# Kernel tuning notes

Measured on AMD Instinct MI355X. Metric: run time of the kernel, lower is better.

## Reference

```python
import jax, jax.numpy as jnp
import numpy as np

N = 2
GRIDS = [(512, 512), (256, 256), (128, 128), (64, 64), (32, 32)]
STRIDES = [4, 8, 16, 32, 64]
SIZES = [32, 64, 128, 256, 512]
ASPECTS = (0.5, 1.0, 2.0)
A = len(ASPECTS)
IMG_H = IMG_W = 2048
PRE_NMS = 1000      # pre_nms_top_n['testing']
POST_NMS = 1000     # post_nms_top_n['testing']
NMS_THRESH = 0.7
SCORE_THRESH = 0.0
MIN_SIZE = 1e-3
BBOX_XFORM_CLIP = float(np.log(1000.0 / 16.0))  # torchvision BoxCoder clamp


def _make_anchors():
    """AnchorGenerator.grid_anchors for each level; returns list of [H*W*A, 4]."""
    ar = jnp.asarray(ASPECTS, jnp.float32)
    hr = jnp.sqrt(ar)
    wr = 1.0 / hr
    levels = []
    for (gh, gw), s, size in zip(GRIDS, STRIDES, SIZES):
        ws = wr * size
        hs = hr * size
        base = jnp.round(jnp.stack([-ws, -hs, ws, hs], 1) / 2.0)  # [A,4]
        sx = (jnp.arange(gw) * s).astype(jnp.float32)
        sy = (jnp.arange(gh) * s).astype(jnp.float32)
        yy, xx = jnp.meshgrid(sy, sx, indexing='ij')
        shifts = jnp.stack([xx.ravel(), yy.ravel(), xx.ravel(), yy.ravel()], 1)
        levels.append((shifts[:, None, :] + base[None, :, :]).reshape(-1, 4))
    return levels


def _flatten_obj(o):
    # permute_and_flatten with C=1: [N,A,H,W] -> [N, H*W*A]
    n, ac, h, w = o.shape
    return o.reshape(n, ac, 1, h, w).transpose(0, 3, 4, 1, 2).reshape(n, -1)


def _flatten_box(b):
    # permute_and_flatten with C=4: [N,A*4,H,W] -> [N, H*W*A, 4]
    n, a4, h, w = b.shape
    return b.reshape(n, a4 // 4, 4, h, w).transpose(0, 3, 4, 1, 2).reshape(n, -1, 4)


def _decode(deltas, anchors):
    # BoxCoder.decode with weights (1,1,1,1); deltas [N,M,4], anchors [M,4]
    wa = anchors[:, 2] - anchors[:, 0]
    ha = anchors[:, 3] - anchors[:, 1]
    cxa = anchors[:, 0] + 0.5 * wa
    cya = anchors[:, 1] + 0.5 * ha
    dx, dy = deltas[..., 0], deltas[..., 1]
    dw = jnp.minimum(deltas[..., 2], BBOX_XFORM_CLIP)
    dh = jnp.minimum(deltas[..., 3], BBOX_XFORM_CLIP)
    cx = dx * wa + cxa
    cy = dy * ha + cya
    w = jnp.exp(dw) * wa
    h = jnp.exp(dh) * ha
    return jnp.stack([cx - 0.5 * w, cy - 0.5 * h, cx + 0.5 * w, cy + 0.5 * h], -1)


def _nms_select(boxes, scores, n_out, thresh):
    """Greedy NMS returning fixed n_out (index, valid) pairs. boxes [K,4]."""
    area = jnp.maximum(boxes[:, 2] - boxes[:, 0], 0.0) * jnp.maximum(boxes[:, 3] - boxes[:, 1], 0.0)

    def step(s, _):
        i = jnp.argmax(s)
        valid = s[i] > -jnp.inf
        b = boxes[i]
        lt = jnp.maximum(boxes[:, :2], b[:2])
        rb = jnp.minimum(boxes[:, 2:], b[2:])
        wh = jnp.maximum(rb - lt, 0.0)
        inter = wh[:, 0] * wh[:, 1]
        iou = inter / (area + area[i] - inter + 1e-9)
        s = jnp.where(iou > thresh, -jnp.inf, s).at[i].set(-jnp.inf)
        return s, (i, valid)

    _, (idx, valid) = jax.lax.scan(step, scores, None, length=n_out)
    return idx, valid


def _rpn_forward(objs, dts):
    anchors = _make_anchors()
    b_all, s_all, l_all = [], [], []
    for li, (o, d, a) in enumerate(zip(objs, dts, anchors)):
        of = _flatten_obj(o)            # [N, HWA]
        df = _flatten_box(d)            # [N, HWA, 4]
        props = _decode(df, a)          # [N, HWA, 4]
        k = min(PRE_NMS, of.shape[1])
        ts, ti = jax.lax.top_k(of, k)   # top-k on raw objectness (per level)
        b_all.append(jnp.take_along_axis(props, ti[..., None], 1))
        s_all.append(ts)
        l_all.append(jnp.full((of.shape[0], k), float(li), jnp.float32))
    boxes = jnp.concatenate(b_all, 1)   # [N, K, 4]
    raw = jnp.concatenate(s_all, 1)     # [N, K]
    lvl = jnp.concatenate(l_all, 1)     # [N, K]

    def per_image(bx, rs, lv):
        sc = jax.nn.sigmoid(rs)
        x1 = jnp.clip(bx[:, 0], 0.0, IMG_W)
        y1 = jnp.clip(bx[:, 1], 0.0, IMG_H)
        x2 = jnp.clip(bx[:, 2], 0.0, IMG_W)
        y2 = jnp.clip(bx[:, 3], 0.0, IMG_H)
        bx = jnp.stack([x1, y1, x2, y2], 1)
        keep = ((x2 - x1) >= MIN_SIZE) & ((y2 - y1) >= MIN_SIZE) & (sc > SCORE_THRESH)
        ms = jnp.where(keep, sc, -jnp.inf)
        off = lv * (IMG_W + IMG_H + 1.0)  # batched_nms level offset
        idx, valid = _nms_select(jax.lax.stop_gradient(bx + off[:, None]),
                                 jax.lax.stop_gradient(ms), POST_NMS, NMS_THRESH)
        v = valid.astype(bx.dtype)
        ob = bx[idx] * v[:, None]
        os = sc[idx] * v
        return jnp.concatenate([ob, os[:, None]], 1)  # [POST_NMS, 5]

    return jax.vmap(per_image)(boxes, raw, lvl)       # [N, POST_NMS, 5]


def setup_inputs() -> dict:
    key = jax.random.key(0)
    ks = jax.random.split(key, 10)
    inp = {}
    for i, (gh, gw) in enumerate(GRIDS):
        inp[f"obj{i}"] = jax.random.normal(ks[i], (N, A, gh, gw), jnp.float32)
        inp[f"box{i}"] = jax.random.normal(ks[5 + i], (N, A * 4, gh, gw), jnp.float32) * 0.5
    return inp


def reference(obj0, obj1, obj2, obj3, obj4, box0, box1, box2, box3, box4):
    return _rpn_forward([obj0, obj1, obj2, obj3, obj4],
                        [box0, box1, box2, box3, box4])
```

## Files before the change

kernel.cpp:

```cpp
#include <hip/hip_runtime.h>
#include <cmath>

#pragma clang fp contract(off)

typedef unsigned int u32;
typedef unsigned short u16;
typedef unsigned long long u64;

#define K_PER_LVL 1000
#define KTOT 5000
#define NIMG 2
#define BINS 16384
#define BIN_SHIFT 18
#define SEGW (BINS / 256)
#define EQ_CAP 2048
#define ECAP 32768
#define LECAP 24576
#define CBUF 1024
#define RNK_IB 512
#define RNK_JB 250
#define RNK_NJ (KTOT / RNK_JB)
#define RNK_TILES 200
#define EDGE_TILES 820

__constant__ int c_LG[5] = {512, 256, 128, 64, 32};
__constant__ int c_LS[5] = {4, 8, 16, 32, 64};
__constant__ int c_LZ[5] = {32, 64, 128, 256, 512};
__constant__ int c_LM[5] = {786432, 196608, 49152, 12288, 3072};

struct Ptrs { const float* o[5]; const float* b[5]; };

__device__ inline u32 fkey(float f) {
    u32 u = __float_as_uint(f);
    return (u & 0x80000000u) ? ~u : (u | 0x80000000u);
}

__device__ inline void featOne(const Ptrs& P, int p, int s, int m,
                               u64* __restrict__ key64, float* __restrict__ csc,
                               float* __restrict__ cbox, float* __restrict__ cobox) {
    int n = p / 5, l = p % 5;
    int G = c_LG[l], S = c_LS[l], Z = c_LZ[l];
    int gg = G * G;
    int a = m % 3; int pix = m / 3; int h = pix / G; int w = pix - h * G;

    const float ars[3] = {0.5f, 1.0f, 2.0f};
    float ar = ars[a];
    float hr = sqrtf(ar), wr = 1.0f / hr;
    float wsz = wr * (float)Z, hsz = hr * (float)Z;
    float bx1 = rintf(-0.5f * wsz), by1 = rintf(-0.5f * hsz);
    float bx2 = rintf(0.5f * wsz),  by2 = rintf(0.5f * hsz);
    float sx = (float)(w * S), sy = (float)(h * S);
    float ax1 = sx + bx1, ay1 = sy + by1, ax2 = sx + bx2, ay2 = sy + by2;
    float wa = ax2 - ax1, ha = ay2 - ay1;
    float cxa = ax1 + 0.5f * wa, cya = ay1 + 0.5f * ha;

    const float* bb = P.b[l] + (size_t)n * 12 * gg;
    float dx = bb[(a * 4 + 0) * gg + pix];
    float dy = bb[(a * 4 + 1) * gg + pix];
    const float CLIPV = 4.135166556742356f;
    float dw = fminf(bb[(a * 4 + 2) * gg + pix], CLIPV);
    float dh = fminf(bb[(a * 4 + 3) * gg + pix], CLIPV);
    float cx = dx * wa + cxa, cy = dy * ha + cya;
    float ww = expf(dw) * wa, hh = expf(dh) * ha;
    float x1 = cx - 0.5f * ww, y1 = cy - 0.5f * hh;
    float x2 = cx + 0.5f * ww, y2 = cy + 0.5f * hh;
    x1 = fminf(fmaxf(x1, 0.f), 2048.f);
    y1 = fminf(fmaxf(y1, 0.f), 2048.f);
    x2 = fminf(fmaxf(x2, 0.f), 2048.f);
    y2 = fminf(fmaxf(y2, 0.f), 2048.f);

    float raw = P.o[l][(size_t)n * 3 * gg + a * gg + pix];
    float sc = 1.0f / (1.0f + expf(-raw));
    bool keep = (x2 - x1 >= 1e-3f) && (y2 - y1 >= 1e-3f) && (sc > 0.0f);

    int slot = n * KTOT + l * K_PER_LVL + s;
    u32 tb = ((u32)l << 20) | (u32)m;
    u32 kk = keep ? fkey(raw) : 0u;
    key64[slot] = ((u64)kk << 23) | (u64)(tb ^ 0x7FFFFFu);

    csc[slot] = keep ? sc : -INFINITY;
    cbox[slot * 4 + 0] = x1; cbox[slot * 4 + 1] = y1;
    cbox[slot * 4 + 2] = x2; cbox[slot * 4 + 3] = y2;
    float off = 4097.0f * (float)l;
    cobox[slot * 4 + 0] = x1 + off; cobox[slot * 4 + 1] = y1 + off;
    cobox[slot * 4 + 2] = x2 + off; cobox[slot * 4 + 3] = y2 + off;
}

__global__ __launch_bounds__(256) void k_zero(u32* __restrict__ z, int nwords) {
    int i = blockIdx.x * 256 + threadIdx.x;
    int stride = gridDim.x * 256;
    for (; i < nwords; i += stride) z[i] = 0;
}

__global__ __launch_bounds__(256) void k_hist(Ptrs P, u32* __restrict__ hist) {
    int p = blockIdx.y; int l = p % 5; int n = p / 5;
    int M4 = c_LM[l] >> 2;
    const float4* base = (const float4*)(P.o[l] + (size_t)n * c_LM[l]);
    __shared__ u32 lh[BINS];
    for (int i = threadIdx.x; i < BINS; i += 256) lh[i] = 0;
    __syncthreads();
    int stride = gridDim.x * 256;
    for (int i = blockIdx.x * 256 + threadIdx.x; i < M4; i += stride) {
        float4 v = base[i];
        atomicAdd(&lh[fkey(v.x) >> BIN_SHIFT], 1u);
        atomicAdd(&lh[fkey(v.y) >> BIN_SHIFT], 1u);
        atomicAdd(&lh[fkey(v.z) >> BIN_SHIFT], 1u);
        atomicAdd(&lh[fkey(v.w) >> BIN_SHIFT], 1u);
    }
    __syncthreads();
    for (int i = threadIdx.x; i < BINS; i += 256) {
        u32 c = lh[i];
        if (c) atomicAdd(&hist[p * BINS + i], c);
    }
}

__global__ __launch_bounds__(256) void k_resolve(const u32* __restrict__ hist,
                                                 int* __restrict__ binB, int* __restrict__ kneed,
                                                 int* __restrict__ g0) {
    int p = blockIdx.x, t = threadIdx.x;
    __shared__ u32 seg[256];
    __shared__ u32 tail[SEGW];
    __shared__ int sgS; __shared__ u32 GS;
    u32 s = 0;
    const u32* hb = hist + p * BINS;
    int base = t * SEGW;
    for (int q = 0; q < SEGW; ++q) s += hb[base + q];
    seg[t] = s;
    __syncthreads();
    if (t == 0) {
        u32 G = 0; int sg = 255;
        for (; sg > 0; --sg) {
            if (G + seg[sg] >= (u32)K_PER_LVL) break;
            G += seg[sg];
        }
        sgS = sg; GS = G;
    }
    __syncthreads();
    int sg = sgS;
    if (t < SEGW) tail[t] = hb[sg * SEGW + t];
    __syncthreads();
    if (t == 0) {
        u32 G = GS; int B = sg * SEGW;
        for (int b = SEGW - 1; b >= 0; --b) {
            u32 c = tail[b];
            if (G + c >= (u32)K_PER_LVL) { B = sg * SEGW + b; break; }
            G += c;
        }
        binB[p] = B;
        kneed[p] = K_PER_LVL - (int)G;
        g0[p] = (int)G;
    }
}

__global__ __launch_bounds__(256) void k_compact(Ptrs P, const int* __restrict__ binB,
                                                 u32* gcnt, u32* ecnt,
                                                 int* __restrict__ sel, u64* __restrict__ eq) {
    int p = blockIdx.y; int l = p % 5; int n = p / 5;
    int M4 = c_LM[l] >> 2; int gg = c_LM[l] / 3;
    const float4* base = (const float4*)(P.o[l] + (size_t)n * c_LM[l]);
    int B = binB[p];
    __shared__ u32 lsel[CBUF];
    __shared__ u64 leq[CBUF];
    __shared__ u32 cSel, cEq, baseSel, baseEq;
    if (threadIdx.x == 0) { cSel = 0; cEq = 0; }
    __syncthreads();
    int stride = gridDim.x * 256;
    for (int i4 = blockIdx.x * 256 + threadIdx.x; i4 < M4; i4 += stride) {
        float4 v = base[i4];
        float vv[4] = {v.x, v.y, v.z, v.w};
        #pragma unroll
        for (int q = 0; q < 4; ++q) {
            u32 k = fkey(vv[q]);
            int bin = (int)(k >> BIN_SHIFT);
            if (bin < B) continue;
            int i = i4 * 4 + q;
            int a = i / gg; int pix = i - a * gg; int m = pix * 3 + a;
            if (bin > B) {
                u32 t = atomicAdd(&cSel, 1u);
                if (t < CBUF) lsel[t] = (u32)m;
                else { u32 pos = atomicAdd(&gcnt[p], 1u); sel[p * K_PER_LVL + pos] = m; }
            } else {
                u64 pk = ((u64)k << 20) | (u64)(0xFFFFFu ^ (u32)m);
                u32 t = atomicAdd(&cEq, 1u);
                if (t < CBUF) leq[t] = pk;
                else { u32 e = atomicAdd(&ecnt[p], 1u); if (e < EQ_CAP) eq[(size_t)p * EQ_CAP + e] = pk; }
            }
        }
    }
    __syncthreads();
    if (threadIdx.x == 0) {
        u32 ns = cSel < CBUF ? cSel : CBUF;
        u32 ne = cEq < CBUF ? cEq : CBUF;
        baseSel = ns ? atomicAdd(&gcnt[p], ns) : 0u;
        baseEq  = ne ? atomicAdd(&ecnt[p], ne) : 0u;
    }
    __syncthreads();
    u32 ns = cSel < CBUF ? cSel : CBUF;
    u32 ne = cEq < CBUF ? cEq : CBUF;
    for (u32 i = threadIdx.x; i < ns; i += 256) sel[p * K_PER_LVL + baseSel + i] = (int)lsel[i];
    for (u32 i = threadIdx.x; i < ne; i += 256) {
        u32 slot = baseEq + i;
        if (slot < EQ_CAP) eq[(size_t)p * EQ_CAP + slot] = leq[i];
    }
}

__global__ __launch_bounds__(256) void k_eqfeat(Ptrs P, const u32* __restrict__ ecnt,
                       const int* __restrict__ kneed, const int* __restrict__ g0,
                       const u64* __restrict__ eq, const int* __restrict__ sel,
                       u64* __restrict__ key64, float* __restrict__ csc,
                       float* __restrict__ cbox, float* __restrict__ cobox) {
    int b = blockIdx.x, t = threadIdx.x;
    if (b < 10) {
        int p = b;
        int E = (int)ecnt[p]; if (E > EQ_CAP) E = EQ_CAP;
        int KF = kneed[p]; int G0 = g0[p];
        __shared__ u64 a[EQ_CAP];
        for (int i = t; i < E; i += 256) a[i] = eq[(size_t)p * EQ_CAP + i];
        __syncthreads();
        u64 mine[8]; int rk[8];
        #pragma unroll
        for (int q = 0; q < 8; ++q) {
            int i = t + q * 256;
            mine[q] = (i < E) ? a[i] : 0ULL;
            rk[q] = 0;
        }
        for (int j = 0; j < E; ++j) {
            u64 v = a[j];
            #pragma unroll
            for (int q = 0; q < 8; ++q) rk[q] += (v > mine[q]) ? 1 : 0;
        }
        #pragma unroll
        for (int q = 0; q < 8; ++q) {
            int i = t + q * 256;
            if (i < E && rk[q] < KF) {
                int m = (int)(0xFFFFFu ^ (u32)(mine[q] & 0xFFFFFu));
                featOne(P, p, G0 + rk[q], m, key64, csc, cbox, cobox);
            }
        }
    } else {
        for (int idx = (b - 10) * 256 + t; idx < 10 * K_PER_LVL; idx += 40 * 256) {
            int p = idx / K_PER_LVL, s = idx - p * K_PER_LVL;
            if (s < g0[p]) featOne(P, p, s, sel[p * K_PER_LVL + s], key64, csc, cbox, cobox);
        }
    }
}

__global__ __launch_bounds__(256) void k_redge(const u64* __restrict__ key64, u32* __restrict__ rpart,
                                               const float* __restrict__ cobox,
                                               u32* __restrict__ gE, u32* __restrict__ gPairs) {
    int n = blockIdx.y;
    int x = blockIdx.x;
    __shared__ u64 kj[RNK_JB];
    __shared__ float cb[64][4];
    if (x < RNK_TILES) {
        int i0 = (x / 20) * RNK_IB;
        int j0 = (x % 20) * RNK_JB;
        const u64* kb = key64 + (size_t)n * KTOT;
        for (int t = threadIdx.x; t < RNK_JB; t += 256) kj[t] = kb[j0 + t];
        __syncthreads();
        int i1 = i0 + threadIdx.x, i2 = i1 + 256;
        u64 k1 = (i1 < KTOT) ? kb[i1] : ~0ULL;
        u64 k2 = (i2 < KTOT) ? kb[i2] : ~0ULL;
        u32 r1 = 0, r2 = 0;
        #pragma unroll 10
        for (int j = 0; j < RNK_JB; ++j) {
            u64 v = kj[j];
            r1 += (v > k1) ? 1u : 0u;
            r2 += (v > k2) ? 1u : 0u;
        }
        u32* rp = rpart + (size_t)(x % 20) * (NIMG * KTOT) + n * KTOT;
        if (i1 < KTOT) rp[i1] = r1;
        if (i2 < KTOT) rp[i2] = r2;
        return;
    }
    int e = x - RNK_TILES, bi = 0;
    while (true) { int c = 79 - 4 * bi; if (e < c) break; e -= c; ++bi; }
    int bj = 4 * bi + e;
    int i = bi * 256 + threadIdx.x;
    int j0 = bj * 64;
    if (threadIdx.x < 64) {
        int jl = j0 + threadIdx.x;
        if (jl < KTOT) {
            cb[threadIdx.x][0] = cobox[(size_t)(n * KTOT + jl) * 4 + 0];
            cb[threadIdx.x][1] = cobox[(size_t)(n * KTOT + jl) * 4 + 1];
            cb[threadIdx.x][2] = cobox[(size_t)(n * KTOT + jl) * 4 + 2];
            cb[threadIdx.x][3] = cobox[(size_t)(n * KTOT + jl) * 4 + 3];
        } else {
            cb[threadIdx.x][0] = 0.f; cb[threadIdx.x][1] = 0.f;
            cb[threadIdx.x][2] = 0.f; cb[threadIdx.x][3] = 0.f;
        }
    }
    __syncthreads();
    if (i >= KTOT) return;
    float x1 = cobox[(size_t)(n * KTOT + i) * 4 + 0];
    float y1 = cobox[(size_t)(n * KTOT + i) * 4 + 1];
    float x2 = cobox[(size_t)(n * KTOT + i) * 4 + 2];
    float y2 = cobox[(size_t)(n * KTOT + i) * 4 + 3];
    float areai = fmaxf(x2 - x1, 0.f) * fmaxf(y2 - y1, 0.f);
    int lim = KTOT - j0; if (lim > 64) lim = 64;
    for (int jj = 0; jj < lim; ++jj) {
        int j = j0 + jj;
        if (j <= i) continue;
        float bx1 = cb[jj][0], by1 = cb[jj][1], bx2 = cb[jj][2], by2 = cb[jj][3];
        float areaj = fmaxf(bx2 - bx1, 0.f) * fmaxf(by2 - by1, 0.f);
        float ltx = fmaxf(x1, bx1), lty = fmaxf(y1, by1);
        float rbx = fminf(x2, bx2), rby = fminf(y2, by2);
        float iw = fmaxf(rbx - ltx, 0.f), ih = fmaxf(rby - lty, 0.f);
        float inter = iw * ih;
        float iou = inter / (areai + areaj - inter + 1e-9f);
        if (iou > 0.7f) {
            u32 pos = atomicAdd(&gE[n], 1u);
            if (pos < ECAP) gPairs[(size_t)n * ECAP + pos] = ((u32)i << 13) | (u32)j;
        }
    }
}

__global__ __launch_bounds__(256) void k_scat(const u32* __restrict__ rpart, const float* __restrict__ csc,
                       const float* __restrict__ cbox,
                       float* __restrict__ ssc, float* __restrict__ sbox, u32* __restrict__ rankArr) {
    int n = blockIdx.y;
    int i = blockIdx.x * 256 + threadIdx.x;
    if (i >= KTOT) return;
    int idx = n * KTOT + i;
    u32 rank = 0;
    #pragma unroll
    for (int jb = 0; jb < RNK_NJ; ++jb) rank += rpart[(size_t)jb * (NIMG * KTOT) + idx];
    rankArr[idx] = rank;
    int src = idx, dst = n * KTOT + (int)rank;
    ssc[dst] = csc[src];
    sbox[dst * 4 + 0] = cbox[src * 4 + 0]; sbox[dst * 4 + 1] = cbox[src * 4 + 1];
    sbox[dst * 4 + 2] = cbox[src * 4 + 2]; sbox[dst * 4 + 3] = cbox[src * 4 + 3];
}

__global__ __launch_bounds__(256, 1) void k_nms(const float* __restrict__ ssc,
                      const float* __restrict__ sbox, const u32* __restrict__ rankArr,
                      const u32* __restrict__ gE, u32* __restrict__ gPairs,
                      u16* __restrict__ gEdges, float* __restrict__ out) {
    int n = blockIdx.x, tid = threadIdx.x;
    int lane = tid & 63, wv = tid >> 6;
    __shared__ u32 cnt[KTOT];
    __shared__ u32 offs[KTOT + 1];
    __shared__ u16 edges[LECAP];
    __shared__ u32 rem32[160];
    __shared__ u32 colLo[64], colHi[64];
    __shared__ u32 scanb[256];
    __shared__ int picksS;

    for (int i = tid; i < KTOT; i += 256) cnt[i] = 0;
    if (tid < 160) rem32[tid] = 0xFFFFFFFFu;
    __syncthreads();
    for (int w = wv; w < 79; w += 4) {
        int i = w * 64 + lane;
        bool dead = (i >= KTOT) || !(ssc[n * KTOT + i] > -INFINITY);
        u64 db = __ballot(dead);
        if (lane == 0) { rem32[2 * w] = (u32)db; rem32[2 * w + 1] = (u32)(db >> 32); }
    }
    __syncthreads();

    int E = (int)gE[n]; if (E > ECAP) E = ECAP;
    for (int k = tid; k < E; k += 256) {
        u32 p = gPairs[(size_t)n * ECAP + k];
        u32 ra = rankArr[n * KTOT + (p >> 13)], rb = rankArr[n * KTOT + (p & 0x1FFFu)];
        u32 src = ra < rb ? ra : rb, dst = ra < rb ? rb : ra;
        gPairs[(size_t)n * ECAP + k] = (src << 13) | dst;
        atomicAdd(&cnt[src], 1u);
    }
    __syncthreads();
    u32 s = 0; int base = tid * 20;
    if (tid < 250) for (int q = 0; q < 20; ++q) s += cnt[base + q];
    scanb[tid] = s;
    __syncthreads();
    for (int off = 1; off < 256; off <<= 1) {
        u32 v = (tid >= off) ? scanb[tid - off] : 0;
        __syncthreads();
        scanb[tid] += v;
        __syncthreads();
    }
    u32 tbase = (tid == 0) ? 0u : scanb[tid - 1];
    if (tid < 250) {
        u32 run = tbase;
        for (int q = 0; q < 20; ++q) { offs[base + q] = run; run += cnt[base + q]; }
    }
    if (tid == 0) offs[KTOT] = scanb[255];
    __syncthreads();
    for (int i = tid; i < KTOT; i += 256) cnt[i] = 0;
    __syncthreads();
    for (int k = tid; k < E; k += 256) {
        u32 p = gPairs[(size_t)n * ECAP + k];
        u32 src = p >> 13, dst = p & 0x1FFFu;
        u32 slot = offs[src] + atomicAdd(&cnt[src], 1u);
        if (slot < LECAP) edges[slot] = (u16)dst;
        else gEdges[(size_t)n * ECAP + slot] = (u16)dst;
    }
    __syncthreads();

    if (wv == 0) {
        int picks = 0;
        for (int w = 0; w < 79 && picks < 1000; ++w) {
            u64 rw = ((u64)rem32[2 * w + 1] << 32) | rem32[2 * w];
            u64 alive = ~rw;
            if (alive == 0ULL) continue;
            int c = w * 64 + lane;
            bool amAlive = ((alive >> lane) & 1ULL) != 0ULL;
            int e0 = 0, e1 = 0;
            if (amAlive) { e0 = (int)offs[c]; e1 = (int)offs[c + 1]; }
            colLo[lane] = 0; colHi[lane] = 0;
            bool anyIntra = false;
            for (int k = e0; k < e1; ++k) {
                int dst = (k < LECAP) ? (int)edges[k] : (int)gEdges[(size_t)n * ECAP + k];
                if ((dst >> 6) == w) {
                    if (lane < 32) atomicOr(&colLo[dst & 63], 1u << lane);
                    else           atomicOr(&colHi[dst & 63], 1u << (lane - 32));
                    anyIntra = true;
                }
            }
            u64 cm;
            if (__ballot(anyIntra) == 0ULL) {
                cm = alive;
            } else {
                u64 col = ((u64)colHi[lane] << 32) | colLo[lane];
                cm = 0ULL;
                u64 remb = alive;
                while (remb) {
                    int e = __builtin_ctzll(remb);
                    remb &= remb - 1ULL;
                    u64 ce = __shfl(col, e);
                    if ((cm & ce) == 0ULL) cm |= (1ULL << e);
                }
            }
            int allowed = 1000 - picks;
            int ncom = __popcll(cm);
            while (ncom > allowed) { cm &= ~(1ULL << (63 - __clzll(cm))); --ncom; }
            if ((cm >> lane) & 1ULL) {
                int pos = picks + (int)__popcll(cm & ((1ULL << lane) - 1ULL));
                const float* bp = &sbox[(size_t)(n * KTOT + c) * 4];
                float* op = &out[(n * 1000 + pos) * 5];
                op[0] = bp[0]; op[1] = bp[1]; op[2] = bp[2]; op[3] = bp[3];
                op[4] = ssc[n * KTOT + c];
                for (int k = e0; k < e1; ++k) {
                    int dst = (k < LECAP) ? (int)edges[k] : (int)gEdges[(size_t)n * ECAP + k];
                    atomicOr(&rem32[dst >> 5], 1u << (dst & 31));
                }
            }
            picks += ncom;
        }
        if (lane == 0) picksS = picks;
    }
    __syncthreads();
    int picksF = picksS;
    int basec = (n * 1000 + picksF) * 5, cntz = (1000 - picksF) * 5;
    for (int t = tid; t < cntz; t += 256) out[basec + t] = 0.f;
}

constexpr size_t OFF_HIST   = 0;
constexpr size_t OFF_GCNT   = OFF_HIST + 10 * BINS * 4;
constexpr size_t OFF_ECNT   = OFF_GCNT + 64;
constexpr size_t OFF_GEC    = OFF_ECNT + 64;
constexpr size_t ZERO_WORDS = (10 * BINS * 4 + 192) / 4;
constexpr size_t OFF_BINB   = OFF_GEC + 64;
constexpr size_t OFF_KNEED  = OFF_BINB + 64;
constexpr size_t OFF_G0     = OFF_KNEED + 64;
constexpr size_t OFF_SEL    = OFF_G0 + 64;
constexpr size_t OFF_EQ     = OFF_SEL + 10 * K_PER_LVL * 4;
constexpr size_t OFF_KEY64  = OFF_EQ + (size_t)10 * EQ_CAP * 8;
constexpr size_t OFF_CSC    = OFF_KEY64 + (size_t)NIMG * KTOT * 8;
constexpr size_t OFF_CBOX   = OFF_CSC + (size_t)NIMG * KTOT * 4;
constexpr size_t OFF_COBOX  = OFF_CBOX + (size_t)NIMG * KTOT * 16;
constexpr size_t OFF_SSC    = OFF_COBOX + (size_t)NIMG * KTOT * 16;
constexpr size_t OFF_SBOX   = OFF_SSC + (size_t)NIMG * KTOT * 4;
constexpr size_t OFF_RANK   = OFF_SBOX + (size_t)NIMG * KTOT * 16;
constexpr size_t OFF_PAIRS  = OFF_RANK + (size_t)NIMG * KTOT * 4;
constexpr size_t OFF_ESPILL = OFF_PAIRS + (size_t)NIMG * ECAP * 4;
constexpr size_t OFF_RPART  = OFF_ESPILL + (size_t)NIMG * ECAP * 2;
constexpr size_t WS_NEEDED  = OFF_RPART + (size_t)RNK_NJ * NIMG * KTOT * 4;

extern "C" void kernel_launch(void* const* d_in, const int* in_sizes, int n_in,
                              void* d_out, int out_size, void* d_ws, size_t ws_size,
                              hipStream_t stream) {
    if (ws_size < WS_NEEDED) return;

    bool dictOrder = (in_sizes[1] > in_sizes[0]);
    Ptrs P;
    for (int l = 0; l < 5; ++l) {
        P.o[l] = (const float*)d_in[dictOrder ? (2 * l)     : l];
        P.b[l] = (const float*)d_in[dictOrder ? (2 * l + 1) : (5 + l)];
    }
    char* ws = (char*)d_ws;
    u32*   hist   = (u32*)(ws + OFF_HIST);
    u32*   gcnt   = (u32*)(ws + OFF_GCNT);
    u32*   ecnt   = (u32*)(ws + OFF_ECNT);
    u32*   gec    = (u32*)(ws + OFF_GEC);
    int*   binB   = (int*)(ws + OFF_BINB);
    int*   kneed  = (int*)(ws + OFF_KNEED);
    int*   g0     = (int*)(ws + OFF_G0);
    int*   sel    = (int*)(ws + OFF_SEL);
    u64*   eq     = (u64*)(ws + OFF_EQ);
    u64*   key64  = (u64*)(ws + OFF_KEY64);
    float* csc    = (float*)(ws + OFF_CSC);
    float* cbox   = (float*)(ws + OFF_CBOX);
    float* cobox  = (float*)(ws + OFF_COBOX);
    float* ssc    = (float*)(ws + OFF_SSC);
    float* sbox   = (float*)(ws + OFF_SBOX);
    u32*   rankA  = (u32*)(ws + OFF_RANK);
    u32*   pairs  = (u32*)(ws + OFF_PAIRS);
    u16*   espill = (u16*)(ws + OFF_ESPILL);
    u32*   rpart  = (u32*)(ws + OFF_RPART);
    float* out    = (float*)d_out;

    k_zero<<<dim3(64), 256, 0, stream>>>(hist, (int)ZERO_WORDS);
    k_hist<<<dim3(32, 10), 256, 0, stream>>>(P, hist);
    k_resolve<<<10, 256, 0, stream>>>(hist, binB, kneed, g0);
    k_compact<<<dim3(64, 10), 256, 0, stream>>>(P, binB, gcnt, ecnt, sel, eq);
    k_eqfeat<<<50, 256, 0, stream>>>(P, ecnt, kneed, g0, eq, sel, key64, csc, cbox, cobox);
    k_redge<<<dim3(RNK_TILES + EDGE_TILES, NIMG), 256, 0, stream>>>(key64, rpart, cobox, gec, pairs);
    k_scat<<<dim3((KTOT + 255) / 256, NIMG), 256, 0, stream>>>(rpart, csc, cbox, ssc, sbox, rankA);
    k_nms<<<NIMG, 256, 0, stream>>>(ssc, sbox, rankA, gec, pairs, espill, out);
}
```

Baseline: 195.9 us.

## Accumulate ranks atomically and drop scatter kernel via inverse permutation in NMS

Rank tiles now atomically add their partial counts into a zeroed rank array instead of writing per-tile partials. This removes the separate k_scat kernel and its partial-rank buffer. k_nms builds an inverse permutation in shared memory and gathers scores and boxes from the unsorted compacted arrays. The change saves one kernel launch and a pass over memory, at the cost of global atomics and indirect gathers inside the single-block-per-image NMS kernel.

```diff
diff --git a/kernel.cpp b/kernel.cpp
--- a/kernel.cpp
+++ b/kernel.cpp
@@ -245,7 +245,7 @@
     }
 }
 
-__global__ __launch_bounds__(256) void k_redge(const u64* __restrict__ key64, u32* __restrict__ rpart,
+__global__ __launch_bounds__(256) void k_redge(const u64* __restrict__ key64, u32* __restrict__ rankArr,
                                                const float* __restrict__ cobox,
                                                u32* __restrict__ gE, u32* __restrict__ gPairs) {
     int n = blockIdx.y;
@@ -268,9 +268,8 @@
             r1 += (v > k1) ? 1u : 0u;
             r2 += (v > k2) ? 1u : 0u;
         }
-        u32* rp = rpart + (size_t)(x % 20) * (NIMG * KTOT) + n * KTOT;
-        if (i1 < KTOT) rp[i1] = r1;
-        if (i2 < KTOT) rp[i2] = r2;
+        if (i1 < KTOT && r1) atomicAdd(&rankArr[n * KTOT + i1], r1);
+        if (i2 < KTOT && r2) atomicAdd(&rankArr[n * KTOT + i2], r2);
         return;
     }
     int e = x - RNK_TILES, bi = 0;
@@ -315,25 +314,8 @@
     }
 }
 
-__global__ __launch_bounds__(256) void k_scat(const u32* __restrict__ rpart, const float* __restrict__ csc,
-                       const float* __restrict__ cbox,
-                       float* __restrict__ ssc, float* __restrict__ sbox, u32* __restrict__ rankArr) {
-    int n = blockIdx.y;
-    int i = blockIdx.x * 256 + threadIdx.x;
-    if (i >= KTOT) return;
-    int idx = n * KTOT + i;
-    u32 rank = 0;
-    #pragma unroll
-    for (int jb = 0; jb < RNK_NJ; ++jb) rank += rpart[(size_t)jb * (NIMG * KTOT) + idx];
-    rankArr[idx] = rank;
-    int src = idx, dst = n * KTOT + (int)rank;
-    ssc[dst] = csc[src];
-    sbox[dst * 4 + 0] = cbox[src * 4 + 0]; sbox[dst * 4 + 1] = cbox[src * 4 + 1];
-    sbox[dst * 4 + 2] = cbox[src * 4 + 2]; sbox[dst * 4 + 3] = cbox[src * 4 + 3];
-}
-
-__global__ __launch_bounds__(256, 1) void k_nms(const float* __restrict__ ssc,
-                      const float* __restrict__ sbox, const u32* __restrict__ rankArr,
+__global__ __launch_bounds__(256, 1) void k_nms(const float* __restrict__ csc,
+                      const float* __restrict__ cbox, const u32* __restrict__ rankArr,
                       const u32* __restrict__ gE, u32* __restrict__ gPairs,
                       u16* __restrict__ gEdges, float* __restrict__ out) {
     int n = blockIdx.x, tid = threadIdx.x;
@@ -341,6 +323,7 @@
     __shared__ u32 cnt[KTOT];
     __shared__ u32 offs[KTOT + 1];
     __shared__ u16 edges[LECAP];
+    __shared__ u16 invL[KTOT];
     __shared__ u32 rem32[160];
     __shared__ u32 colLo[64], colHi[64];
     __shared__ u32 scanb[256];
@@ -348,10 +331,11 @@
 
     for (int i = tid; i < KTOT; i += 256) cnt[i] = 0;
     if (tid < 160) rem32[tid] = 0xFFFFFFFFu;
+    for (int i = tid; i < KTOT; i += 256) invL[rankArr[n * KTOT + i]] = (u16)i;
     __syncthreads();
     for (int w = wv; w < 79; w += 4) {
         int i = w * 64 + lane;
-        bool dead = (i >= KTOT) || !(ssc[n * KTOT + i] > -INFINITY);
+        bool dead = (i >= KTOT) || !(csc[n * KTOT + (int)invL[i]] > -INFINITY);
         u64 db = __ballot(dead);
         if (lane == 0) { rem32[2 * w] = (u32)db; rem32[2 * w + 1] = (u32)(db >> 32); }
     }
@@ -433,10 +417,11 @@
             while (ncom > allowed) { cm &= ~(1ULL << (63 - __clzll(cm))); --ncom; }
             if ((cm >> lane) & 1ULL) {
                 int pos = picks + (int)__popcll(cm & ((1ULL << lane) - 1ULL));
-                const float* bp = &sbox[(size_t)(n * KTOT + c) * 4];
+                int orig = (int)invL[c];
+                const float* bp = &cbox[(size_t)(n * KTOT + orig) * 4];
                 float* op = &out[(n * 1000 + pos) * 5];
                 op[0] = bp[0]; op[1] = bp[1]; op[2] = bp[2]; op[3] = bp[3];
-                op[4] = ssc[n * KTOT + c];
+                op[4] = csc[n * KTOT + orig];
                 for (int k = e0; k < e1; ++k) {
                     int dst = (k < LECAP) ? (int)edges[k] : (int)gEdges[(size_t)n * ECAP + k];
                     atomicOr(&rem32[dst >> 5], 1u << (dst & 31));
@@ -456,8 +441,9 @@
 constexpr size_t OFF_GCNT   = OFF_HIST + 10 * BINS * 4;
 constexpr size_t OFF_ECNT   = OFF_GCNT + 64;
 constexpr size_t OFF_GEC    = OFF_ECNT + 64;
-constexpr size_t ZERO_WORDS = (10 * BINS * 4 + 192) / 4;
-constexpr size_t OFF_BINB   = OFF_GEC + 64;
+constexpr size_t OFF_RANK   = OFF_GEC + 64;
+constexpr size_t ZERO_WORDS = (10 * BINS * 4 + 192 + (size_t)NIMG * KTOT * 4) / 4;
+constexpr size_t OFF_BINB   = OFF_RANK + (size_t)NIMG * KTOT * 4;
 constexpr size_t OFF_KNEED  = OFF_BINB + 64;
 constexpr size_t OFF_G0     = OFF_KNEED + 64;
 constexpr size_t OFF_SEL    = OFF_G0 + 64;
@@ -466,13 +452,9 @@
 constexpr size_t OFF_CSC    = OFF_KEY64 + (size_t)NIMG * KTOT * 8;
 constexpr size_t OFF_CBOX   = OFF_CSC + (size_t)NIMG * KTOT * 4;
 constexpr size_t OFF_COBOX  = OFF_CBOX + (size_t)NIMG * KTOT * 16;
-constexpr size_t OFF_SSC    = OFF_COBOX + (size_t)NIMG * KTOT * 16;
-constexpr size_t OFF_SBOX   = OFF_SSC + (size_t)NIMG * KTOT * 4;
-constexpr size_t OFF_RANK   = OFF_SBOX + (size_t)NIMG * KTOT * 16;
-constexpr size_t OFF_PAIRS  = OFF_RANK + (size_t)NIMG * KTOT * 4;
+constexpr size_t OFF_PAIRS  = OFF_COBOX + (size_t)NIMG * KTOT * 16;
 constexpr size_t OFF_ESPILL = OFF_PAIRS + (size_t)NIMG * ECAP * 4;
-constexpr size_t OFF_RPART  = OFF_ESPILL + (size_t)NIMG * ECAP * 2;
-constexpr size_t WS_NEEDED  = OFF_RPART + (size_t)RNK_NJ * NIMG * KTOT * 4;
+constexpr size_t WS_NEEDED  = OFF_ESPILL + (size_t)NIMG * ECAP * 2;
 
 extern "C" void kernel_launch(void* const* d_in, const int* in_sizes, int n_in,
                               void* d_out, int out_size, void* d_ws, size_t ws_size,
@@ -490,6 +472,7 @@
     u32*   gcnt   = (u32*)(ws + OFF_GCNT);
     u32*   ecnt   = (u32*)(ws + OFF_ECNT);
     u32*   gec    = (u32*)(ws + OFF_GEC);
+    u32*   rankA  = (u32*)(ws + OFF_RANK);
     int*   binB   = (int*)(ws + OFF_BINB);
     int*   kneed  = (int*)(ws + OFF_KNEED);
     int*   g0     = (int*)(ws + OFF_G0);
@@ -499,12 +482,8 @@
     float* csc    = (float*)(ws + OFF_CSC);
     float* cbox   = (float*)(ws + OFF_CBOX);
     float* cobox  = (float*)(ws + OFF_COBOX);
-    float* ssc    = (float*)(ws + OFF_SSC);
-    float* sbox   = (float*)(ws + OFF_SBOX);
-    u32*   rankA  = (u32*)(ws + OFF_RANK);
     u32*   pairs  = (u32*)(ws + OFF_PAIRS);
     u16*   espill = (u16*)(ws + OFF_ESPILL);
-    u32*   rpart  = (u32*)(ws + OFF_RPART);
     float* out    = (float*)d_out;
 
     k_zero<<<dim3(64), 256, 0, stream>>>(hist, (int)ZERO_WORDS);
@@ -512,7 +491,6 @@
     k_resolve<<<10, 256, 0, stream>>>(hist, binB, kneed, g0);
     k_compact<<<dim3(64, 10), 256, 0, stream>>>(P, binB, gcnt, ecnt, sel, eq);
     k_eqfeat<<<50, 256, 0, stream>>>(P, ecnt, kneed, g0, eq, sel, key64, csc, cbox, cobox);
-    k_redge<<<dim3(RNK_TILES + EDGE_TILES, NIMG), 256, 0, stream>>>(key64, rpart, cobox, gec, pairs);
-    k_scat<<<dim3((KTOT + 255) / 256, NIMG), 256, 0, stream>>>(rpart, csc, cbox, ssc, sbox, rankA);
-    k_nms<<<NIMG, 256, 0, stream>>>(ssc, sbox, rankA, gec, pairs, espill, out);
-}
+    k_redge<<<dim3(RNK_TILES + EDGE_TILES, NIMG), 256, 0, stream>>>(key64, rankA, cobox, gec, pairs);
+    k_nms<<<NIMG, 256, 0, stream>>>(csc, cbox, rankA, gec, pairs, espill, out);
+}
```

New measurement: 193.6 us. No clear change (-1.2%).
